# Kernel optimization log

Hardware: AMD Instinct MI355X
Metric: run time of the kernel (lower is better)

The kernel has to match this reference:

```python
import jax, jax.numpy as jnp
import numpy as np

EPS = 1e-20


def _conv(x, w, pad):
    # NCHW / OIHW conv, stride 1, symmetric padding
    return jax.lax.conv_general_dilated(
        x, w, window_strides=(1, 1),
        padding=((pad, pad), (pad, pad)),
        dimension_numbers=("NCHW", "OIHW", "NCHW"))


def _nconv(data, conf, w, b, pad):
    # normalized convolution: conv(d*c)/conv(c) + bias ; cout = conv(c)/sum(w)
    denom = _conv(conf, w, pad)
    nomin = _conv(data * conf, w, pad)
    out = nomin / (denom + EPS) + b[None, :, None, None]
    s = jnp.sum(w, axis=(1, 2, 3))  # per-out-channel kernel sum
    cout = denom / s[None, :, None, None]
    return out, cout


def _maxpool_ds(x, c):
    # 2x2/stride-2 max pool on c, gathering x at argmax positions (torch return_indices semantics)
    B, C, H, W = c.shape
    cw = c.reshape(B, C, H // 2, 2, W // 2, 2).transpose(0, 1, 2, 4, 3, 5).reshape(B, C, H // 2, W // 2, 4)
    xw = x.reshape(B, C, H // 2, 2, W // 2, 2).transpose(0, 1, 2, 4, 3, 5).reshape(B, C, H // 2, W // 2, 4)
    idx = jnp.argmax(cw, axis=-1)  # first-max tie-break, same as torch
    c_ds = jnp.take_along_axis(cw, idx[..., None], axis=-1)[..., 0] / 4.0
    x_ds = jnp.take_along_axis(xw, idx[..., None], axis=-1)[..., 0]
    return x_ds, c_ds


def _up2(x):
    return jnp.repeat(jnp.repeat(x, 2, axis=2), 2, axis=3)


def setup_inputs() -> dict:
    key = jax.random.key(0)
    ks = jax.random.split(key, 18)
    B, H, W = 8, 512, 512
    x0 = jax.random.normal(ks[0], (B, 1, H, W), dtype=jnp.float32)
    c0 = jax.random.uniform(ks[1], (B, 1, H, W), dtype=jnp.float32)

    def posw(k, shape):
        # positive kernel (the module enforces positivity via softplus hook)
        return jax.nn.softplus(jax.random.normal(k, shape, dtype=jnp.float32))

    inp = {"x0": x0, "c0": c0}
    shapes = {
        "w1": (2, 1, 5, 5), "w2": (2, 2, 5, 5), "w3": (2, 2, 5, 5),
        "w4": (2, 4, 3, 3), "w5": (2, 4, 3, 3), "w6": (2, 4, 3, 3),
        "w7": (1, 2, 1, 1),
    }
    for i, (name, shp) in enumerate(shapes.items()):
        inp[name] = posw(ks[2 + i], shp)
        inp["b" + name[1:]] = jnp.full((shp[0],), 0.01, dtype=jnp.float32)
    return inp


def reference(x0, c0, w1, b1, w2, b2, w3, b3, w4, b4, w5, b5, w6, b6, w7, b7):
    x1, c1 = _nconv(x0, c0, w1, b1, 2)
    x1, c1 = _nconv(x1, c1, w2, b2, 2)
    x1, c1 = _nconv(x1, c1, w3, b3, 2)

    x1_ds, c1_ds = _maxpool_ds(x1, c1)
    x2_ds, c2_ds = _nconv(x1_ds, c1_ds, w2, b2, 2)
    x2_ds, c2_ds = _nconv(x2_ds, c2_ds, w3, b3, 2)

    x2_dss, c2_dss = _maxpool_ds(x2_ds, c2_ds)
    x3_ds, c3_ds = _nconv(x2_dss, c2_dss, w2, b2, 2)

    x3_dss, c3_dss = _maxpool_ds(x3_ds, c3_ds)
    x4_ds, c4_ds = _nconv(x3_dss, c3_dss, w2, b2, 2)

    x4, c4 = _up2(x4_ds), _up2(c4_ds)
    x34_ds, c34_ds = _nconv(jnp.concatenate((x3_ds, x4), 1), jnp.concatenate((c3_ds, c4), 1), w4, b4, 1)

    x34, c34 = _up2(x34_ds), _up2(c34_ds)
    x23_ds, c23_ds = _nconv(jnp.concatenate((x2_ds, x34), 1), jnp.concatenate((c2_ds, c34), 1), w5, b5, 1)

    x23, c23 = _up2(x23_ds), _up2(c23_ds)
    xout, cout = _nconv(jnp.concatenate((x23, x1), 1), jnp.concatenate((c23, c1), 1), w6, b6, 1)
    xout, cout = _nconv(xout, cout, w7, b7, 0)
    return xout, cout
```

## Files before the change

### kernel.cpp

```cpp
#include <hip/hip_runtime.h>

#define EPSF 1e-20f

__device__ __forceinline__ float frcp(float x) { return __builtin_amdgcn_rcpf(x); }


template<int NCI, int CI0, int CINT, int K, int ROWS>
__device__ __forceinline__ void conv_core(const float* __restrict__ s_d,
                                          const float* __restrict__ s_c,
                                          const float* __restrict__ wgt,
                                          int lh, int lw,
                                          float den[2][4], float nom[2][4])
{
    constexpr int JOFF = 4 - (K / 2);
    #pragma unroll
    for (int kh = 0; kh < K; ++kh) {
        #pragma unroll
        for (int ci = 0; ci < NCI; ++ci) {
            const float2* rd = (const float2*)(s_d + (ci * ROWS + lh + kh) * 72 + lw + 2);
            const float2* rc = (const float2*)(s_c + (ci * ROWS + lh + kh) * 72 + lw + 2);
            float wd[8], wc[8];
            #pragma unroll
            for (int q = 0; q < 4; ++q) {
                const float2 t = rd[q];
                wd[2*q] = t.x; wd[2*q+1] = t.y;
                const float2 u = rc[q];
                wc[2*q] = u.x; wc[2*q+1] = u.y;
            }
            #pragma unroll
            for (int kw = 0; kw < K; ++kw) {
                const float w0 = wgt[((0 * CINT + CI0 + ci) * K + kh) * K + kw];
                const float w1 = wgt[((1 * CINT + CI0 + ci) * K + kh) * K + kw];
                #pragma unroll
                for (int p = 0; p < 4; ++p) {
                    const int j = p + kw + (JOFF - 2);
                    den[0][p] = fmaf(w0, wc[j], den[0][p]);
                    nom[0][p] = fmaf(w0, wd[j], nom[0][p]);
                    den[1][p] = fmaf(w1, wc[j], den[1][p]);
                    nom[1][p] = fmaf(w1, wd[j], nom[1][p]);
                }
            }
        }
    }
}

template<int LO0>
__device__ __forceinline__ void conv_low(const float* __restrict__ s_lo_d,
                                         const float* __restrict__ s_lo_c,
                                         const float* __restrict__ wgt,
                                         int lh, int lw,
                                         float den[2][4], float nom[2][4])
{
    #pragma unroll
    for (int kh = 0; kh < 3; ++kh) {
        const int rel_r = ((lh + kh - 1) >> 1) + 1;
        #pragma unroll
        for (int lci = 0; lci < 2; ++lci) {
            const float* rd = s_lo_d + (lci * 10 + rel_r) * 40 + (lw >> 1) + 2;
            const float* rc = s_lo_c + (lci * 10 + rel_r) * 40 + (lw >> 1) + 2;
            float wd[6], wc[6];
            #pragma unroll
            for (int q = 0; q < 3; ++q) {
                const float2 t = *(const float2*)(rd + 2 * q);
                wd[2*q] = t.x; wd[2*q+1] = t.y;
                const float2 u = *(const float2*)(rc + 2 * q);
                wc[2*q] = u.x; wc[2*q+1] = u.y;
            }
            #pragma unroll
            for (int kw = 0; kw < 3; ++kw) {
                const float w0 = wgt[((0 * 4 + LO0 + lci) * 3 + kh) * 3 + kw];
                const float w1 = wgt[((1 * 4 + LO0 + lci) * 3 + kh) * 3 + kw];
                #pragma unroll
                for (int p = 0; p < 4; ++p) {
                    const int t = p + kw - 1;
                    const int jl = ((t < 0) ? -1 : (t >> 1)) + 2;
                    den[0][p] = fmaf(w0, wc[jl], den[0][p]);
                    nom[0][p] = fmaf(w0, wd[jl], nom[0][p]);
                    den[1][p] = fmaf(w1, wc[jl], den[1][p]);
                    nom[1][p] = fmaf(w1, wd[jl], nom[1][p]);
                }
            }
        }
    }
}

template<int CINT, int K>
__device__ __forceinline__ void nconv_epilogue(const float* __restrict__ wgt,
                                               const float* __restrict__ bias,
                                               float den[2][4], float nom[2][4],
                                               float4 uo[2], float4 co4[2])
{
    #pragma unroll
    for (int c = 0; c < 2; ++c) {
        float s = 0.f;
        for (int i = 0; i < CINT * K * K; ++i) s += wgt[c * CINT * K * K + i];
        const float is = 1.0f / s;
        const float bb = bias[c];
        #pragma unroll
        for (int p = 0; p < 4; ++p) {
            const float xo = nom[c][p] * frcp(den[c][p] + EPSF) + bb;
            const float cv = den[c][p] * is;
            (&co4[c].x)[p] = cv;
            (&uo[c].x)[p]  = xo * cv;
        }
    }
}

__global__ __launch_bounds__(256)
void enc12_fused(const float* __restrict__ x0, const float* __restrict__ c0,
                 const float* __restrict__ wA, const float* __restrict__ bA,
                 const float* __restrict__ wB, const float* __restrict__ bB,
                 float* __restrict__ uout, float* __restrict__ cout)
{
    __shared__ __align__(16) float in_d[24][84], in_c[24][84];
    __shared__ __align__(16) float mid_d[2][20][72], mid_c[2][20][72];

    const int tid = threadIdx.x;
    const int bw = blockIdx.x * 64;
    const int bh = blockIdx.y * 16;
    const int b  = blockIdx.z;

    const float4* x4 = (const float4*)x0;
    const float4* c4 = (const float4*)c0;
    for (int i = tid; i < 480; i += 256) {
        const int r = i / 20, k = i % 20;
        const int gh = bh - 4 + r;
        const int gw4 = (bw >> 2) - 2 + k;
        float4 xx = make_float4(0.f, 0.f, 0.f, 0.f);
        float4 cc = make_float4(0.f, 0.f, 0.f, 0.f);
        if ((unsigned)gh < 512u && (unsigned)gw4 < 128u) {
            const int a = (b << 16) + (gh << 7) + gw4;
            xx = x4[a];
            cc = c4[a];
        }
        *(float4*)&in_d[r][4 * k] = make_float4(xx.x * cc.x, xx.y * cc.y, xx.z * cc.z, xx.w * cc.w);
        *(float4*)&in_c[r][4 * k] = cc;
    }

    float isA0, isA1;
    {
        float s0 = 0.f, s1 = 0.f;
        for (int i = 0; i < 25; ++i) { s0 += wA[i]; s1 += wA[25 + i]; }
        isA0 = 1.0f / s0;
        isA1 = 1.0f / s1;
    }
    __syncthreads();

    #pragma unroll
    for (int pass = 0; pass < 2; ++pass) {
        int r, g;
        bool active = true;
        if (pass == 0) { r = tid >> 4; g = tid & 15; }
        else {
            if (tid < 64) { r = 16 + (tid >> 4); g = tid & 15; }
            else if (tid < 104) { const int t = tid - 64; r = t >> 1; g = 16 + (t & 1); }
            else { active = false; r = 0; g = 0; }
        }
        if (active) {
            float den[2][4], nom[2][4];
            #pragma unroll
            for (int c = 0; c < 2; ++c)
                #pragma unroll
                for (int p = 0; p < 4; ++p) { den[c][p] = 0.f; nom[c][p] = 0.f; }
            #pragma unroll
            for (int kh = 0; kh < 5; ++kh) {
                const float2* rd = (const float2*)(&in_d[r + kh][4 * g + 2]);
                const float2* rc = (const float2*)(&in_c[r + kh][4 * g + 2]);
                float wd[8], wc[8];
                #pragma unroll
                for (int q = 0; q < 4; ++q) {
                    const float2 t = rd[q];
                    wd[2*q] = t.x; wd[2*q+1] = t.y;
                    const float2 u = rc[q];
                    wc[2*q] = u.x; wc[2*q+1] = u.y;
                }
                #pragma unroll
                for (int kw = 0; kw < 5; ++kw) {
                    const float w0 = wA[kh * 5 + kw];
                    const float w1 = wA[25 + kh * 5 + kw];
                    #pragma unroll
                    for (int p = 0; p < 4; ++p) {
                        const int m = p + kw;
                        den[0][p] = fmaf(w0, wc[m], den[0][p]);
                        nom[0][p] = fmaf(w0, wd[m], nom[0][p]);
                        den[1][p] = fmaf(w1, wc[m], den[1][p]);
                        nom[1][p] = fmaf(w1, wd[m], nom[1][p]);
                    }
                }
            }
            const int orow = bh + r - 2;
            const bool rok = (unsigned)orow < 512u;
            #pragma unroll
            for (int c = 0; c < 2; ++c) {
                const float is = (c == 0) ? isA0 : isA1;
                float4 du, dc;
                #pragma unroll
                for (int p = 0; p < 4; ++p) {
                    const int ocol = bw + 4 * g - 4 + p;
                    const bool ok = rok && (unsigned)ocol < 512u;
                    const float xo = nom[c][p] * frcp(den[c][p] + EPSF) + bA[c];
                    const float cv = den[c][p] * is;
                    (&dc.x)[p] = ok ? cv : 0.f;
                    (&du.x)[p] = ok ? xo * cv : 0.f;
                }
                *(float4*)&mid_d[c][r][4 * g] = du;
                *(float4*)&mid_c[c][r][4 * g] = dc;
            }
        }
    }
    __syncthreads();

    const int lh = tid >> 4;
    const int lw = (tid & 15) << 2;
    float den[2][4], nom[2][4];
    #pragma unroll
    for (int c = 0; c < 2; ++c)
        #pragma unroll
        for (int p = 0; p < 4; ++p) { den[c][p] = 0.f; nom[c][p] = 0.f; }

    conv_core<2, 0, 2, 5, 20>(&mid_d[0][0][0], &mid_c[0][0][0], wB, lh, lw, den, nom);

    float4 uo[2], co4[2];
    nconv_epilogue<2, 5>(wB, bB, den, nom, uo, co4);

    const int oh = bh + lh;
    #pragma unroll
    for (int c = 0; c < 2; ++c) {
        const int a = ((b * 2 + c) << 16) + (oh << 7) + ((bw + lw) >> 2);
        ((float4*)uout)[a] = uo[c];
        ((float4*)cout)[a] = co4[c];
    }
}

__global__ __launch_bounds__(256)
void enc45_fused(const float* __restrict__ inU, const float* __restrict__ inC,
                 const float* __restrict__ wA, const float* __restrict__ bA,
                 const float* __restrict__ wB, const float* __restrict__ bB,
                 float* __restrict__ uout, float* __restrict__ cout,
                 float* __restrict__ poolU, float* __restrict__ poolC)
{
    __shared__ __align__(16) float in_d[2][24][84], in_c[2][24][84];
    __shared__ __align__(16) float mid_d[2][20][72], mid_c[2][20][72];

    const int tid = threadIdx.x;
    const int bw = blockIdx.x * 64;
    const int bh = blockIdx.y * 16;
    const int b  = blockIdx.z;

    const float4* U4 = (const float4*)inU;
    const float4* C4 = (const float4*)inC;
    for (int i = tid; i < 960; i += 256) {
        const int ci = i / 480;
        const int r = (i / 20) % 24, k = i % 20;
        const int gh = bh - 4 + r;
        const int gw4 = (bw >> 2) - 2 + k;
        float4 dd = make_float4(0.f, 0.f, 0.f, 0.f);
        float4 cc = make_float4(0.f, 0.f, 0.f, 0.f);
        if ((unsigned)gh < 256u && (unsigned)gw4 < 64u) {
            const int a = ((b * 2 + ci) << 14) + (gh << 6) + gw4;
            dd = U4[a];
            cc = C4[a];
        }
        *(float4*)&in_d[ci][r][4 * k] = dd;
        *(float4*)&in_c[ci][r][4 * k] = cc;
    }

    float isA0, isA1;
    {
        float s0 = 0.f, s1 = 0.f;
        for (int i = 0; i < 50; ++i) { s0 += wA[i]; s1 += wA[50 + i]; }
        isA0 = 1.0f / s0;
        isA1 = 1.0f / s1;
    }
    __syncthreads();

    #pragma unroll
    for (int pass = 0; pass < 2; ++pass) {
        int r, g;
        bool active = true;
        if (pass == 0) { r = tid >> 4; g = tid & 15; }
        else {
            if (tid < 64) { r = 16 + (tid >> 4); g = tid & 15; }
            else if (tid < 104) { const int t = tid - 64; r = t >> 1; g = 16 + (t & 1); }
            else { active = false; r = 0; g = 0; }
        }
        if (active) {
            float den[2][4], nom[2][4];
            #pragma unroll
            for (int c = 0; c < 2; ++c)
                #pragma unroll
                for (int p = 0; p < 4; ++p) { den[c][p] = 0.f; nom[c][p] = 0.f; }
            #pragma unroll
            for (int kh = 0; kh < 5; ++kh) {
                #pragma unroll
                for (int ci = 0; ci < 2; ++ci) {
                    const float2* rd = (const float2*)(&in_d[ci][r + kh][4 * g + 2]);
                    const float2* rc = (const float2*)(&in_c[ci][r + kh][4 * g + 2]);
                    float wd[8], wc[8];
                    #pragma unroll
                    for (int q = 0; q < 4; ++q) {
                        const float2 t = rd[q];
                        wd[2*q] = t.x; wd[2*q+1] = t.y;
                        const float2 u = rc[q];
                        wc[2*q] = u.x; wc[2*q+1] = u.y;
                    }
                    #pragma unroll
                    for (int kw = 0; kw < 5; ++kw) {
                        const float w0 = wA[((0 * 2 + ci) * 5 + kh) * 5 + kw];
                        const float w1 = wA[((1 * 2 + ci) * 5 + kh) * 5 + kw];
                        #pragma unroll
                        for (int p = 0; p < 4; ++p) {
                            const int m = p + kw;
                            den[0][p] = fmaf(w0, wc[m], den[0][p]);
                            nom[0][p] = fmaf(w0, wd[m], nom[0][p]);
                            den[1][p] = fmaf(w1, wc[m], den[1][p]);
                            nom[1][p] = fmaf(w1, wd[m], nom[1][p]);
                        }
                    }
                }
            }
            const int orow = bh + r - 2;
            const bool rok = (unsigned)orow < 256u;
            #pragma unroll
            for (int c = 0; c < 2; ++c) {
                const float is = (c == 0) ? isA0 : isA1;
                float4 du, dc;
                #pragma unroll
                for (int p = 0; p < 4; ++p) {
                    const int ocol = bw + 4 * g - 4 + p;
                    const bool ok = rok && (unsigned)ocol < 256u;
                    const float xo = nom[c][p] * frcp(den[c][p] + EPSF) + bA[c];
                    const float cv = den[c][p] * is;
                    (&dc.x)[p] = ok ? cv : 0.f;
                    (&du.x)[p] = ok ? xo * cv : 0.f;
                }
                *(float4*)&mid_d[c][r][4 * g] = du;
                *(float4*)&mid_c[c][r][4 * g] = dc;
            }
        }
    }
    __syncthreads();

    const int lh = tid >> 4;
    const int lw = (tid & 15) << 2;
    float den[2][4], nom[2][4];
    #pragma unroll
    for (int c = 0; c < 2; ++c)
        #pragma unroll
        for (int p = 0; p < 4; ++p) { den[c][p] = 0.f; nom[c][p] = 0.f; }

    conv_core<2, 0, 2, 5, 20>(&mid_d[0][0][0], &mid_c[0][0][0], wB, lh, lw, den, nom);

    float4 uo[2], co4[2];
    nconv_epilogue<2, 5>(wB, bB, den, nom, uo, co4);

    const int oh = bh + lh;
    #pragma unroll
    for (int c = 0; c < 2; ++c) {
        const int a = ((b * 2 + c) << 14) + (oh << 6) + ((bw + lw) >> 2);
        ((float4*)uout)[a] = uo[c];
        ((float4*)cout)[a] = co4[c];
    }

    __syncthreads();
    float* pu = &mid_d[0][0][0];
    float* pcb = &mid_c[0][0][0];
    #pragma unroll
    for (int c = 0; c < 2; ++c) {
        *(float4*)&pu[(c * 16 + lh) * 64 + lw] = uo[c];
        *(float4*)&pcb[(c * 16 + lh) * 64 + lw] = co4[c];
    }
    __syncthreads();
    #pragma unroll
    for (int rep = 0; rep < 2; ++rep) {
        const int o = tid + rep * 256;
        const int ch = o >> 8;
        const int idx = o & 255;
        const int pr = idx >> 5;
        const int pcc = idx & 31;
        const int bse = (ch * 16 + 2 * pr) * 64 + 2 * pcc;
        const float c00 = pcb[bse],      c01 = pcb[bse + 1];
        const float c10 = pcb[bse + 64], c11 = pcb[bse + 65];
        float m = c00; float g = pu[bse];
        if (c01 > m) { m = c01; g = pu[bse + 1]; }
        if (c10 > m) { m = c10; g = pu[bse + 64]; }
        if (c11 > m) { m = c11; g = pu[bse + 65]; }
        const int pa = ((b * 2 + ch) << 14) + (((bh >> 1) + pr) << 7) + (bw >> 1) + pcc;
        poolU[pa] = g * 0.25f;
        poolC[pa] = m * 0.25f;
    }
}

__global__ __launch_bounds__(256)
void mid_kern(const float* __restrict__ p2U, const float* __restrict__ p2C,
              const float* __restrict__ w2, const float* __restrict__ b2,
              const float* __restrict__ w4, const float* __restrict__ b4,
              float* __restrict__ x34U, float* __restrict__ x34C)
{
    __shared__ __align__(16) float sp_d[2][32][88], sp_c[2][32][88];
    __shared__ __align__(16) float sx3_d[2][28][80], sx3_c[2][28][80];
    __shared__ __align__(16) float sp3_d[2][14][48], sp3_c[2][14][48];
    __shared__ __align__(16) float sx4_d[2][10][40], sx4_c[2][10][40];

    const int tid = threadIdx.x;
    const int bw = blockIdx.x * 64;
    const int bh = blockIdx.y * 16;
    const int b = blockIdx.z;

    const float4* U4 = (const float4*)p2U;
    const float4* C4 = (const float4*)p2C;
    for (int i = tid; i < 2 * 32 * 22; i += 256) {
        const int ci = i / 704;
        const int r  = (i / 22) % 32;
        const int cf = i % 22;
        const int gh = bh - 8 + r;
        const int gw4 = (bw >> 2) - 3 + cf;
        float4 dd = make_float4(0.f, 0.f, 0.f, 0.f);
        float4 cc = make_float4(0.f, 0.f, 0.f, 0.f);
        if ((unsigned)gh < 128u && (unsigned)gw4 < 32u) {
            const int a = ((b * 2 + ci) << 12) + (gh << 5) + gw4;
            dd = U4[a];
            cc = C4[a];
        }
        *(float4*)&sp_d[ci][r][cf * 4] = dd;
        *(float4*)&sp_c[ci][r][cf * 4] = cc;
    }
    __syncthreads();

    {
        float s2[2];
        #pragma unroll
        for (int c = 0; c < 2; ++c) {
            float s = 0.f;
            for (int i = 0; i < 50; ++i) s += w2[c * 50 + i];
            s2[c] = 1.0f / s;
        }
        for (int s = tid; s < 560; s += 256) {
            const int r = s / 20;
            const int g = s % 20;
            float den[2][4], nom[2][4];
            #pragma unroll
            for (int c = 0; c < 2; ++c)
                #pragma unroll
                for (int p = 0; p < 4; ++p) { den[c][p] = 0.f; nom[c][p] = 0.f; }
            #pragma unroll
            for (int kh = 0; kh < 5; ++kh) {
                #pragma unroll
                for (int ci = 0; ci < 2; ++ci) {
                    const float2* rd = (const float2*)(&sp_d[ci][r + kh][4 * g + 2]);
                    const float2* rc = (const float2*)(&sp_c[ci][r + kh][4 * g + 2]);
                    float wd[8], wc[8];
                    #pragma unroll
                    for (int q = 0; q < 4; ++q) {
                        const float2 t = rd[q];
                        wd[2*q] = t.x; wd[2*q+1] = t.y;
                        const float2 u = rc[q];
                        wc[2*q] = u.x; wc[2*q+1] = u.y;
                    }
                    #pragma unroll
                    for (int kw = 0; kw < 5; ++kw) {
                        const float w0 = w2[((0 * 2 + ci) * 5 + kh) * 5 + kw];
                        const float w1 = w2[((1 * 2 + ci) * 5 + kh) * 5 + kw];
                        #pragma unroll
                        for (int p = 0; p < 4; ++p) {
                            const int j = p + kw;
                            den[0][p] = fmaf(w0, wc[j], den[0][p]);
                            nom[0][p] = fmaf(w0, wd[j], nom[0][p]);
                            den[1][p] = fmaf(w1, wc[j], den[1][p]);
                            nom[1][p] = fmaf(w1, wd[j], nom[1][p]);
                        }
                    }
                }
            }
            const int orow = bh - 6 + r;
            const bool rok = (unsigned)orow < 128u;
            #pragma unroll
            for (int c = 0; c < 2; ++c) {
                float4 du, dc;
                #pragma unroll
                for (int p = 0; p < 4; ++p) {
                    const int ocol = bw - 8 + 4 * g + p;
                    const bool ok = rok && (unsigned)ocol < 128u;
                    const float xo = nom[c][p] * frcp(den[c][p] + EPSF) + b2[c];
                    const float cv = den[c][p] * s2[c];
                    (&dc.x)[p] = ok ? cv : 0.f;
                    (&du.x)[p] = ok ? xo * cv : 0.f;
                }
                *(float4*)&sx3_d[c][r][4 * g] = du;
                *(float4*)&sx3_c[c][r][4 * g] = dc;
            }
        }
    }
    __syncthreads();

    for (int i = tid; i < 2 * 14 * 48; i += 256) {
        const int ch = i / 672;
        const int r  = (i / 48) % 14;
        const int c  = i % 48;
        const int R = (bh >> 1) - 3 + r;
        const int C = (bw >> 1) - 8 + c;
        float g = 0.f, m = 0.f;
        if (c >= 4 && c < 44 && (unsigned)R < 64u && (unsigned)C < 64u) {
            const int xr = 2 * r, xc = 2 * c - 8;
            const float c00 = sx3_c[ch][xr][xc],     c01 = sx3_c[ch][xr][xc + 1];
            const float c10 = sx3_c[ch][xr + 1][xc], c11 = sx3_c[ch][xr + 1][xc + 1];
            m = c00; g = sx3_d[ch][xr][xc];
            if (c01 > m) { m = c01; g = sx3_d[ch][xr][xc + 1]; }
            if (c10 > m) { m = c10; g = sx3_d[ch][xr + 1][xc]; }
            if (c11 > m) { m = c11; g = sx3_d[ch][xr + 1][xc + 1]; }
            g *= 0.25f; m *= 0.25f;
        }
        sp3_d[ch][r][c] = g;
        sp3_c[ch][r][c] = m;
    }
    __syncthreads();

    {
        float s2[2];
        #pragma unroll
        for (int c = 0; c < 2; ++c) {
            float s = 0.f;
            for (int i = 0; i < 50; ++i) s += w2[c * 50 + i];
            s2[c] = 1.0f / s;
        }
        for (int s = tid; s < 100; s += 256) {
            const int r = s / 10;
            const int g = s % 10;
            float den[2][4], nom[2][4];
            #pragma unroll
            for (int c = 0; c < 2; ++c)
                #pragma unroll
                for (int p = 0; p < 4; ++p) { den[c][p] = 0.f; nom[c][p] = 0.f; }
            #pragma unroll
            for (int kh = 0; kh < 5; ++kh) {
                #pragma unroll
                for (int ci = 0; ci < 2; ++ci) {
                    const float2* rd = (const float2*)(&sp3_d[ci][r + kh][4 * g + 2]);
                    const float2* rc = (const float2*)(&sp3_c[ci][r + kh][4 * g + 2]);
                    float wd[8], wc[8];
                    #pragma unroll
                    for (int q = 0; q < 4; ++q) {
                        const float2 t = rd[q];
                        wd[2*q] = t.x; wd[2*q+1] = t.y;
                        const float2 u = rc[q];
                        wc[2*q] = u.x; wc[2*q+1] = u.y;
                    }
                    #pragma unroll
                    for (int kw = 0; kw < 5; ++kw) {
                        const float w0 = w2[((0 * 2 + ci) * 5 + kh) * 5 + kw];
                        const float w1 = w2[((1 * 2 + ci) * 5 + kh) * 5 + kw];
                        #pragma unroll
                        for (int p = 0; p < 4; ++p) {
                            const int j = p + kw;
                            den[0][p] = fmaf(w0, wc[j], den[0][p]);
                            nom[0][p] = fmaf(w0, wd[j], nom[0][p]);
                            den[1][p] = fmaf(w1, wc[j], den[1][p]);
                            nom[1][p] = fmaf(w1, wd[j], nom[1][p]);
                        }
                    }
                }
            }
            const int orow = (bh >> 1) - 1 + r;
            const bool rok = (unsigned)orow < 64u;
            #pragma unroll
            for (int c = 0; c < 2; ++c) {
                float4 du, dc;
                #pragma unroll
                for (int p = 0; p < 4; ++p) {
                    const int ocol = (bw >> 1) - 4 + 4 * g + p;
                    const bool ok = rok && (unsigned)ocol < 64u;
                    const float xo = nom[c][p] * frcp(den[c][p] + EPSF) + b2[c];
                    const float cv = den[c][p] * s2[c];
                    (&dc.x)[p] = ok ? cv : 0.f;
                    (&du.x)[p] = ok ? xo * cv : 0.f;
                }
                *(float4*)&sx4_d[c][r][4 * g] = du;
                *(float4*)&sx4_c[c][r][4 * g] = dc;
            }
        }
    }
    __syncthreads();

    {
        const int lh = tid >> 4;
        const int lw = (tid & 15) << 2;
        float den[2][4], nom[2][4];
        #pragma unroll
        for (int c = 0; c < 2; ++c)
            #pragma unroll
            for (int p = 0; p < 4; ++p) { den[c][p] = 0.f; nom[c][p] = 0.f; }

        #pragma unroll
        for (int kh = 0; kh < 3; ++kh) {
            #pragma unroll
            for (int ci = 0; ci < 2; ++ci) {
                const float2* rd = (const float2*)(&sx3_d[ci][lh + kh + 5][lw + 6]);
                const float2* rc = (const float2*)(&sx3_c[ci][lh + kh + 5][lw + 6]);
                float wd[8], wc[8];
                #pragma unroll
                for (int q = 0; q < 4; ++q) {
                    const float2 t = rd[q];
                    wd[2*q] = t.x; wd[2*q+1] = t.y;
                    const float2 u = rc[q];
                    wc[2*q] = u.x; wc[2*q+1] = u.y;
                }
                #pragma unroll
                for (int kw = 0; kw < 3; ++kw) {
                    const float w0 = w4[((0 * 4 + ci) * 3 + kh) * 3 + kw];
                    const float w1 = w4[((1 * 4 + ci) * 3 + kh) * 3 + kw];
                    #pragma unroll
                    for (int p = 0; p < 4; ++p) {
                        const int j = p + kw + 1;
                        den[0][p] = fmaf(w0, wc[j], den[0][p]);
                        nom[0][p] = fmaf(w0, wd[j], nom[0][p]);
                        den[1][p] = fmaf(w1, wc[j], den[1][p]);
                        nom[1][p] = fmaf(w1, wd[j], nom[1][p]);
                    }
                }
            }
        }
        conv_low<2>(&sx4_d[0][0][0], &sx4_c[0][0][0], w4, lh, lw, den, nom);

        float4 uo[2], co4[2];
        nconv_epilogue<4, 3>(w4, b4, den, nom, uo, co4);
        #pragma unroll
        for (int c = 0; c < 2; ++c) {
            const int a = ((b * 2 + c) << 12) + ((bh + lh) << 5) + ((bw + lw) >> 2);
            ((float4*)x34U)[a] = uo[c];
            ((float4*)x34C)[a] = co4[c];
        }
    }
}

template<int CIN, int K, int LOGHW, bool IN_IS_U, bool POOL>
__global__ __launch_bounds__(256)
void nconv_tiled(const float* __restrict__ xin, const float* __restrict__ cin_,
                 const float* __restrict__ wgt, const float* __restrict__ bias,
                 float* __restrict__ uout, float* __restrict__ cout,
                 float* __restrict__ poolU, float* __restrict__ poolC)
{
    constexpr int HW = 1 << LOGHW;
    constexpr int PAD = K / 2;
    constexpr int TH = 16;
    constexpr int ROWS = TH + 2 * PAD;
    constexpr int NC4 = 18;
    __shared__ __align__(16) float s_d[CIN][ROWS][72];
    __shared__ __align__(16) float s_c[CIN][ROWS][72];

    const int tid = threadIdx.x;
    const int base_w = blockIdx.x * 64;
    const int base_h = blockIdx.y * TH;
    const int b = blockIdx.z;

    constexpr int SLOTS = CIN * ROWS * NC4;
    const float4* x4 = (const float4*)xin;
    const float4* c4p = (const float4*)cin_;
    for (int i = tid; i < SLOTS; i += 256) {
        const int ci = i / (ROWS * NC4);
        const int r  = (i / NC4) % ROWS;
        const int cf = i % NC4;
        const int gh = base_h - PAD + r;
        const int gw4 = (base_w >> 2) + cf - 1;
        float4 dd = make_float4(0.f, 0.f, 0.f, 0.f);
        float4 cc = make_float4(0.f, 0.f, 0.f, 0.f);
        if ((unsigned)gh < (unsigned)HW && (unsigned)gw4 < (unsigned)(HW >> 2)) {
            const int a = ((b * CIN + ci) << (2 * LOGHW - 2)) + (gh << (LOGHW - 2)) + gw4;
            const float4 xx = x4[a];
            cc = c4p[a];
            if (IN_IS_U) dd = xx;
            else dd = make_float4(xx.x * cc.x, xx.y * cc.y, xx.z * cc.z, xx.w * cc.w);
        }
        *(float4*)&s_d[ci][r][cf * 4] = dd;
        *(float4*)&s_c[ci][r][cf * 4] = cc;
    }
    __syncthreads();

    const int lh = tid >> 4;
    const int lw = (tid & 15) << 2;
    float den[2][4], nom[2][4];
    #pragma unroll
    for (int c = 0; c < 2; ++c)
        #pragma unroll
        for (int p = 0; p < 4; ++p) { den[c][p] = 0.f; nom[c][p] = 0.f; }

    conv_core<CIN, 0, CIN, K, ROWS>(&s_d[0][0][0], &s_c[0][0][0], wgt, lh, lw, den, nom);

    float4 uo[2], co4[2];
    nconv_epilogue<CIN, K>(wgt, bias, den, nom, uo, co4);

    const int oh = base_h + lh;
    #pragma unroll
    for (int c = 0; c < 2; ++c) {
        const int a = ((b * 2 + c) << (2 * LOGHW - 2)) + (oh << (LOGHW - 2)) + ((base_w + lw) >> 2);
        ((float4*)uout)[a] = uo[c];
        ((float4*)cout)[a] = co4[c];
    }

    if (POOL) {
        __syncthreads();
        float* pu = &s_d[0][0][0];
        float* pcb = &s_c[0][0][0];
        #pragma unroll
        for (int c = 0; c < 2; ++c) {
            *(float4*)&pu[(c * 16 + lh) * 64 + lw] = uo[c];
            *(float4*)&pcb[(c * 16 + lh) * 64 + lw] = co4[c];
        }
        __syncthreads();
        #pragma unroll
        for (int rep = 0; rep < 2; ++rep) {
            const int o = tid + rep * 256;
            const int ch = o >> 8;
            const int idx = o & 255;
            const int pr = idx >> 5;
            const int pcc = idx & 31;
            const int bse = (ch * 16 + 2 * pr) * 64 + 2 * pcc;
            const float c00 = pcb[bse],      c01 = pcb[bse + 1];
            const float c10 = pcb[bse + 64], c11 = pcb[bse + 65];
            float m = c00; float g = pu[bse];
            if (c01 > m) { m = c01; g = pu[bse + 1]; }
            if (c10 > m) { m = c10; g = pu[bse + 64]; }
            if (c11 > m) { m = c11; g = pu[bse + 65]; }
            const int pa = ((b * 2 + ch) << (2 * (LOGHW - 1)))
                         + (((base_h >> 1) + pr) << (LOGHW - 1)) + (base_w >> 1) + pcc;
            poolU[pa] = g * 0.25f;
            poolC[pa] = m * 0.25f;
        }
    }
}

template<bool UP_FIRST, int LOGHW, bool FINAL>
__global__ __launch_bounds__(256)
void nconv_cat_tiled(const float* __restrict__ skU, const float* __restrict__ skC,
                     const float* __restrict__ loU, const float* __restrict__ loC,
                     const float* __restrict__ wgt, const float* __restrict__ bias,
                     float* __restrict__ uout, float* __restrict__ cout,
                     const float* __restrict__ w7, const float* __restrict__ b7)
{
    constexpr int HW = 1 << LOGHW;
    constexpr int HWL = HW >> 1;
    constexpr int TH = 16;
    constexpr int ROWS = TH + 2;
    constexpr int NC4 = 18;
    constexpr int SK0 = UP_FIRST ? 2 : 0;
    constexpr int LO0 = UP_FIRST ? 0 : 2;
    __shared__ __align__(16) float s_d[2][ROWS][72];
    __shared__ __align__(16) float s_c[2][ROWS][72];
    __shared__ __align__(16) float s_lo_d[2][10][40];
    __shared__ __align__(16) float s_lo_c[2][10][40];

    const int tid = threadIdx.x;
    const int base_w = blockIdx.x * 64;
    const int base_h = blockIdx.y * TH;
    const int b = blockIdx.z;

    constexpr int SLOTS = 2 * ROWS * NC4;
    const float4* sU4 = (const float4*)skU;
    const float4* sC4 = (const float4*)skC;
    for (int i = tid; i < SLOTS; i += 256) {
        const int ci = i / (ROWS * NC4);
        const int r  = (i / NC4) % ROWS;
        const int cf = i % NC4;
        const int gh = base_h - 1 + r;
        const int gw4 = (base_w >> 2) + cf - 1;
        float4 dd = make_float4(0.f, 0.f, 0.f, 0.f);
        float4 cc = make_float4(0.f, 0.f, 0.f, 0.f);
        if ((unsigned)gh < (unsigned)HW && (unsigned)gw4 < (unsigned)(HW >> 2)) {
            const int a = ((b * 2 + ci) << (2 * LOGHW - 2)) + (gh << (LOGHW - 2)) + gw4;
            dd = sU4[a];
            cc = sC4[a];
        }
        *(float4*)&s_d[ci][r][cf * 4] = dd;
        *(float4*)&s_c[ci][r][cf * 4] = cc;
    }
    constexpr int LO_SLOTS = 2 * 10 * 10;
    const int lo_r0 = (base_h >> 1) - 1;
    const int lo_c4_0 = (base_w >> 3) - 1;
    const float4* lU4 = (const float4*)loU;
    const float4* lC4 = (const float4*)loC;
    for (int i = tid; i < LO_SLOTS; i += 256) {
        const int ci = i / 100;
        const int r  = (i / 10) % 10;
        const int cf = i % 10;
        const int gr = lo_r0 + r;
        const int gc4 = lo_c4_0 + cf;
        float4 dd = make_float4(0.f, 0.f, 0.f, 0.f);
        float4 cc = make_float4(0.f, 0.f, 0.f, 0.f);
        if ((unsigned)gr < (unsigned)HWL && (unsigned)gc4 < (unsigned)(HWL >> 2)) {
            const int a = ((b * 2 + ci) << (2 * (LOGHW - 1) - 2)) + (gr << (LOGHW - 3)) + gc4;
            dd = lU4[a];
            cc = lC4[a];
        }
        *(float4*)&s_lo_d[ci][r][cf * 4] = dd;
        *(float4*)&s_lo_c[ci][r][cf * 4] = cc;
    }
    __syncthreads();

    const int lh = tid >> 4;
    const int lw = (tid & 15) << 2;
    float den[2][4], nom[2][4];
    #pragma unroll
    for (int c = 0; c < 2; ++c)
        #pragma unroll
        for (int p = 0; p < 4; ++p) { den[c][p] = 0.f; nom[c][p] = 0.f; }

    conv_core<2, SK0, 4, 3, ROWS>(&s_d[0][0][0], &s_c[0][0][0], wgt, lh, lw, den, nom);
    conv_low<LO0>(&s_lo_d[0][0][0], &s_lo_c[0][0][0], wgt, lh, lw, den, nom);

    float4 uo[2], co4[2];
    nconv_epilogue<4, 3>(wgt, bias, den, nom, uo, co4);

    const int oh = base_h + lh;
    if (FINAL) {
        const float w70 = w7[0], w71 = w7[1], bb7 = b7[0];
        const float inv = frcp(w70 + w71);
        float4 xo4, cc4;
        #pragma unroll
        for (int p = 0; p < 4; ++p) {
            const float d1 = w70 * (&co4[0].x)[p] + w71 * (&co4[1].x)[p];
            (&xo4.x)[p] = (w70 * (&uo[0].x)[p] + w71 * (&uo[1].x)[p]) * frcp(d1 + EPSF) + bb7;
            (&cc4.x)[p] = d1 * inv;
        }
        const int a = (b << (2 * LOGHW - 2)) + (oh << (LOGHW - 2)) + ((base_w + lw) >> 2);
        ((float4*)uout)[a] = xo4;
        ((float4*)uout)[(1 << 19) + a] = cc4;
    } else {
        #pragma unroll
        for (int c = 0; c < 2; ++c) {
            const int a = ((b * 2 + c) << (2 * LOGHW - 2)) + (oh << (LOGHW - 2)) + ((base_w + lw) >> 2);
            ((float4*)uout)[a] = uo[c];
            ((float4*)cout)[a] = co4[c];
        }
    }
}

extern "C" void kernel_launch(void* const* d_in, const int* in_sizes, int n_in,
                              void* d_out, int out_size, void* d_ws, size_t ws_size,
                              hipStream_t stream) {
    (void)in_sizes; (void)n_in; (void)out_size; (void)ws_size;
    const float* x0 = (const float*)d_in[0];
    const float* c0 = (const float*)d_in[1];
    const float* w1 = (const float*)d_in[2];  const float* b1 = (const float*)d_in[3];
    const float* w2 = (const float*)d_in[4];  const float* b2 = (const float*)d_in[5];
    const float* w3 = (const float*)d_in[6];  const float* b3 = (const float*)d_in[7];
    const float* w4 = (const float*)d_in[8];  const float* b4 = (const float*)d_in[9];
    const float* w5 = (const float*)d_in[10]; const float* b5 = (const float*)d_in[11];
    const float* w6 = (const float*)d_in[12]; const float* b6 = (const float*)d_in[13];
    const float* w7 = (const float*)d_in[14]; const float* b7 = (const float*)d_in[15];

    float* ws = (float*)d_ws;
    const size_t S512 = 8ull * 2 * 512 * 512;
    const size_t S256 = 8ull * 2 * 256 * 256;
    const size_t S128 = 8ull * 2 * 128 * 128;

    float* X1x = ws;            float* X1c = ws + S512;
    float* Ax  = ws + 2 * S512; float* Ac  = ws + 3 * S512;
    float* Bx  = ws + 4 * S512; float* Bc  = ws + 5 * S512;
    float* x23x = Ax;               float* x23c = Ax + S256;
    float* x2x  = Ax + 2 * S256;    float* x2c  = Ax + 3 * S256;
    float* p1x  = Ax + 4 * S256;    float* p1c  = Ax + 5 * S256;
    float* p2x  = Bx + 2 * S128;    float* p2c  = Bx + 3 * S128;
    float* x34x = Bx + 4 * S128;    float* x34c = Bx + 5 * S128;

    enc12_fused<<<dim3(8, 32, 8), 256, 0, stream>>>(
        x0, c0, w1, b1, w2, b2, Bx, Bc);
    nconv_tiled<2, 5, 9, true, true><<<dim3(8, 32, 8), 256, 0, stream>>>(
        Bx, Bc, w3, b3, X1x, X1c, p1x, p1c);
    enc45_fused<<<dim3(4, 16, 8), 256, 0, stream>>>(
        p1x, p1c, w2, b2, w3, b3, x2x, x2c, p2x, p2c);
    mid_kern<<<dim3(2, 8, 8), 256, 0, stream>>>(
        p2x, p2c, w2, b2, w4, b4, x34x, x34c);
    nconv_cat_tiled<false, 8, false><<<dim3(4, 16, 8), 256, 0, stream>>>(
        x2x, x2c, x34x, x34c, w5, b5, x23x, x23c, nullptr, nullptr);
    nconv_cat_tiled<true, 9, true><<<dim3(8, 32, 8), 256, 0, stream>>>(
        X1x, X1c, x23x, x23c, w6, b6, (float*)d_out, nullptr, w7, b7);
}
```

Before: 142.1 us.

## Interleave confidence and data into float2 shared-memory tiles across all conv kernels

Replaces the separate shared-memory arrays for confidence and confidence-weighted data with one interleaved float2 array per tile. Window loads become four 16-byte LDS reads per row instead of eight 8-byte reads, and accumulators are kept as float2 pairs (den, nom), which may let the compiler emit packed FMA. The pooling stage also reads interleaved pairs. Shared-memory footprint is unchanged, but bank-conflict patterns and register allocation shift, so occupancy may change.

```diff
diff --git a/kernel.cpp b/kernel.cpp
--- a/kernel.cpp
+++ b/kernel.cpp
@@ -5,39 +5,53 @@
 __device__ __forceinline__ float frcp(float x) { return __builtin_amdgcn_rcpf(x); }
 
 
+struct CD8 { float2 v[8]; };
+__device__ __forceinline__ CD8 load_cd8(const float2* p) {
+    const float4* q = (const float4*)p;
+    const float4 t0 = q[0], t1 = q[1], t2 = q[2], t3 = q[3];
+    CD8 r;
+    r.v[0] = make_float2(t0.x, t0.y); r.v[1] = make_float2(t0.z, t0.w);
+    r.v[2] = make_float2(t1.x, t1.y); r.v[3] = make_float2(t1.z, t1.w);
+    r.v[4] = make_float2(t2.x, t2.y); r.v[5] = make_float2(t2.z, t2.w);
+    r.v[6] = make_float2(t3.x, t3.y); r.v[7] = make_float2(t3.z, t3.w);
+    return r;
+}
+struct CD6 { float2 v[6]; };
+__device__ __forceinline__ CD6 load_cd6(const float2* p) {
+    const float4* q = (const float4*)p;
+    const float4 t0 = q[0], t1 = q[1], t2 = q[2];
+    CD6 r;
+    r.v[0] = make_float2(t0.x, t0.y); r.v[1] = make_float2(t0.z, t0.w);
+    r.v[2] = make_float2(t1.x, t1.y); r.v[3] = make_float2(t1.z, t1.w);
+    r.v[4] = make_float2(t2.x, t2.y); r.v[5] = make_float2(t2.z, t2.w);
+    return r;
+}
+__device__ __forceinline__ void fma2(float2& a, float w, float2 cd) {
+    a.x = fmaf(w, cd.x, a.x);
+    a.y = fmaf(w, cd.y, a.y);
+}
+
 template<int NCI, int CI0, int CINT, int K, int ROWS>
-__device__ __forceinline__ void conv_core(const float* __restrict__ s_d,
-                                          const float* __restrict__ s_c,
-                                          const float* __restrict__ wgt,
-                                          int lh, int lw,
-                                          float den[2][4], float nom[2][4])
+__device__ __forceinline__ void conv_core_i(const float2* __restrict__ s,
+                                            const float* __restrict__ wgt,
+                                            int lh, int lw,
+                                            float2 acc[2][4])
 {
-    constexpr int JOFF = 4 - (K / 2);
+    constexpr int JB = 2 - (K / 2);
     #pragma unroll
     for (int kh = 0; kh < K; ++kh) {
         #pragma unroll
         for (int ci = 0; ci < NCI; ++ci) {
-            const float2* rd = (const float2*)(s_d + (ci * ROWS + lh + kh) * 72 + lw + 2);
-            const float2* rc = (const float2*)(s_c + (ci * ROWS + lh + kh) * 72 + lw + 2);
-            float wd[8], wc[8];
-            #pragma unroll
-            for (int q = 0; q < 4; ++q) {
-                const float2 t = rd[q];
-                wd[2*q] = t.x; wd[2*q+1] = t.y;
-                const float2 u = rc[q];
-                wc[2*q] = u.x; wc[2*q+1] = u.y;
-            }
+            const CD8 cd = load_cd8(s + (ci * ROWS + lh + kh) * 72 + lw + 2);
             #pragma unroll
             for (int kw = 0; kw < K; ++kw) {
                 const float w0 = wgt[((0 * CINT + CI0 + ci) * K + kh) * K + kw];
                 const float w1 = wgt[((1 * CINT + CI0 + ci) * K + kh) * K + kw];
                 #pragma unroll
                 for (int p = 0; p < 4; ++p) {
-                    const int j = p + kw + (JOFF - 2);
-                    den[0][p] = fmaf(w0, wc[j], den[0][p]);
-                    nom[0][p] = fmaf(w0, wd[j], nom[0][p]);
-                    den[1][p] = fmaf(w1, wc[j], den[1][p]);
-                    nom[1][p] = fmaf(w1, wd[j], nom[1][p]);
+                    const int j = p + kw + JB;
+                    fma2(acc[0][p], w0, cd.v[j]);
+                    fma2(acc[1][p], w1, cd.v[j]);
                 }
             }
         }
@@ -45,27 +59,17 @@
 }
 
 template<int LO0>
-__device__ __forceinline__ void conv_low(const float* __restrict__ s_lo_d,
-                                         const float* __restrict__ s_lo_c,
-                                         const float* __restrict__ wgt,
-                                         int lh, int lw,
-                                         float den[2][4], float nom[2][4])
+__device__ __forceinline__ void conv_low_i(const float2* __restrict__ s_lo,
+                                           const float* __restrict__ wgt,
+                                           int lh, int lw,
+                                           float2 acc[2][4])
 {
     #pragma unroll
     for (int kh = 0; kh < 3; ++kh) {
         const int rel_r = ((lh + kh - 1) >> 1) + 1;
         #pragma unroll
         for (int lci = 0; lci < 2; ++lci) {
-            const float* rd = s_lo_d + (lci * 10 + rel_r) * 40 + (lw >> 1) + 2;
-            const float* rc = s_lo_c + (lci * 10 + rel_r) * 40 + (lw >> 1) + 2;
-            float wd[6], wc[6];
-            #pragma unroll
-            for (int q = 0; q < 3; ++q) {
-                const float2 t = *(const float2*)(rd + 2 * q);
-                wd[2*q] = t.x; wd[2*q+1] = t.y;
-                const float2 u = *(const float2*)(rc + 2 * q);
-                wc[2*q] = u.x; wc[2*q+1] = u.y;
-            }
+            const CD6 cd = load_cd6(s_lo + (lci * 10 + rel_r) * 40 + (lw >> 1) + 2);
             #pragma unroll
             for (int kw = 0; kw < 3; ++kw) {
                 const float w0 = wgt[((0 * 4 + LO0 + lci) * 3 + kh) * 3 + kw];
@@ -74,10 +78,8 @@
                 for (int p = 0; p < 4; ++p) {
                     const int t = p + kw - 1;
                     const int jl = ((t < 0) ? -1 : (t >> 1)) + 2;
-                    den[0][p] = fmaf(w0, wc[jl], den[0][p]);
-                    nom[0][p] = fmaf(w0, wd[jl], nom[0][p]);
-                    den[1][p] = fmaf(w1, wc[jl], den[1][p]);
-                    nom[1][p] = fmaf(w1, wd[jl], nom[1][p]);
+                    fma2(acc[0][p], w0, cd.v[jl]);
+                    fma2(acc[1][p], w1, cd.v[jl]);
                 }
             }
         }
@@ -85,10 +87,10 @@
 }
 
 template<int CINT, int K>
-__device__ __forceinline__ void nconv_epilogue(const float* __restrict__ wgt,
-                                               const float* __restrict__ bias,
-                                               float den[2][4], float nom[2][4],
-                                               float4 uo[2], float4 co4[2])
+__device__ __forceinline__ void nconv_epilogue_i(const float* __restrict__ wgt,
+                                                 const float* __restrict__ bias,
+                                                 float2 acc[2][4],
+                                                 float4 uo[2], float4 co4[2])
 {
     #pragma unroll
     for (int c = 0; c < 2; ++c) {
@@ -98,8 +100,8 @@
         const float bb = bias[c];
         #pragma unroll
         for (int p = 0; p < 4; ++p) {
-            const float xo = nom[c][p] * frcp(den[c][p] + EPSF) + bb;
-            const float cv = den[c][p] * is;
+            const float xo = acc[c][p].y * frcp(acc[c][p].x + EPSF) + bb;
+            const float cv = acc[c][p].x * is;
             (&co4[c].x)[p] = cv;
             (&uo[c].x)[p]  = xo * cv;
         }
@@ -112,8 +114,8 @@
                  const float* __restrict__ wB, const float* __restrict__ bB,
                  float* __restrict__ uout, float* __restrict__ cout)
 {
-    __shared__ __align__(16) float in_d[24][84], in_c[24][84];
-    __shared__ __align__(16) float mid_d[2][20][72], mid_c[2][20][72];
+    __shared__ __align__(16) float2 in_cd[24][84];
+    __shared__ __align__(16) float2 mid_cd[2][20][72];
 
     const int tid = threadIdx.x;
     const int bw = blockIdx.x * 64;
@@ -133,8 +135,9 @@
             xx = x4[a];
             cc = c4[a];
         }
-        *(float4*)&in_d[r][4 * k] = make_float4(xx.x * cc.x, xx.y * cc.y, xx.z * cc.z, xx.w * cc.w);
-        *(float4*)&in_c[r][4 * k] = cc;
+        float4* dst = (float4*)&in_cd[r][4 * k];
+        dst[0] = make_float4(cc.x, xx.x * cc.x, cc.y, xx.y * cc.y);
+        dst[1] = make_float4(cc.z, xx.z * cc.z, cc.w, xx.w * cc.w);
     }
 
     float isA0, isA1;
@@ -157,34 +160,22 @@
             else { active = false; r = 0; g = 0; }
         }
         if (active) {
-            float den[2][4], nom[2][4];
+            float2 acc[2][4];
             #pragma unroll
             for (int c = 0; c < 2; ++c)
                 #pragma unroll
-                for (int p = 0; p < 4; ++p) { den[c][p] = 0.f; nom[c][p] = 0.f; }
+                for (int p = 0; p < 4; ++p) acc[c][p] = make_float2(0.f, 0.f);
             #pragma unroll
             for (int kh = 0; kh < 5; ++kh) {
-                const float2* rd = (const float2*)(&in_d[r + kh][4 * g + 2]);
-                const float2* rc = (const float2*)(&in_c[r + kh][4 * g + 2]);
-                float wd[8], wc[8];
-                #pragma unroll
-                for (int q = 0; q < 4; ++q) {
-                    const float2 t = rd[q];
-                    wd[2*q] = t.x; wd[2*q+1] = t.y;
-                    const float2 u = rc[q];
-                    wc[2*q] = u.x; wc[2*q+1] = u.y;
-                }
+                const CD8 cd = load_cd8(&in_cd[r + kh][4 * g + 2]);
                 #pragma unroll
                 for (int kw = 0; kw < 5; ++kw) {
                     const float w0 = wA[kh * 5 + kw];
                     const float w1 = wA[25 + kh * 5 + kw];
                     #pragma unroll
                     for (int p = 0; p < 4; ++p) {
-                        const int m = p + kw;
-                        den[0][p] = fmaf(w0, wc[m], den[0][p]);
-                        nom[0][p] = fmaf(w0, wd[m], nom[0][p]);
-                        den[1][p] = fmaf(w1, wc[m], den[1][p]);
-                        nom[1][p] = fmaf(w1, wd[m], nom[1][p]);
+                        fma2(acc[0][p], w0, cd.v[p + kw]);
+                        fma2(acc[1][p], w1, cd.v[p + kw]);
                     }
                 }
             }
@@ -193,18 +184,19 @@
             #pragma unroll
             for (int c = 0; c < 2; ++c) {
                 const float is = (c == 0) ? isA0 : isA1;
-                float4 du, dc;
+                float cv[4], du[4];
                 #pragma unroll
                 for (int p = 0; p < 4; ++p) {
                     const int ocol = bw + 4 * g - 4 + p;
                     const bool ok = rok && (unsigned)ocol < 512u;
-                    const float xo = nom[c][p] * frcp(den[c][p] + EPSF) + bA[c];
-                    const float cv = den[c][p] * is;
-                    (&dc.x)[p] = ok ? cv : 0.f;
-                    (&du.x)[p] = ok ? xo * cv : 0.f;
-                }
-                *(float4*)&mid_d[c][r][4 * g] = du;
-                *(float4*)&mid_c[c][r][4 * g] = dc;
+                    const float xo = acc[c][p].y * frcp(acc[c][p].x + EPSF) + bA[c];
+                    const float v = acc[c][p].x * is;
+                    cv[p] = ok ? v : 0.f;
+                    du[p] = ok ? xo * v : 0.f;
+                }
+                float4* dst = (float4*)&mid_cd[c][r][4 * g];
+                dst[0] = make_float4(cv[0], du[0], cv[1], du[1]);
+                dst[1] = make_float4(cv[2], du[2], cv[3], du[3]);
             }
         }
     }
@@ -212,16 +204,16 @@
 
     const int lh = tid >> 4;
     const int lw = (tid & 15) << 2;
-    float den[2][4], nom[2][4];
+    float2 acc[2][4];
     #pragma unroll
     for (int c = 0; c < 2; ++c)
         #pragma unroll
-        for (int p = 0; p < 4; ++p) { den[c][p] = 0.f; nom[c][p] = 0.f; }
-
-    conv_core<2, 0, 2, 5, 20>(&mid_d[0][0][0], &mid_c[0][0][0], wB, lh, lw, den, nom);
+        for (int p = 0; p < 4; ++p) acc[c][p] = make_float2(0.f, 0.f);
+
+    conv_core_i<2, 0, 2, 5, 20>(&mid_cd[0][0][0], wB, lh, lw, acc);
 
     float4 uo[2], co4[2];
-    nconv_epilogue<2, 5>(wB, bB, den, nom, uo, co4);
+    nconv_epilogue_i<2, 5>(wB, bB, acc, uo, co4);
 
     const int oh = bh + lh;
     #pragma unroll
@@ -239,8 +231,8 @@
                  float* __restrict__ uout, float* __restrict__ cout,
                  float* __restrict__ poolU, float* __restrict__ poolC)
 {
-    __shared__ __align__(16) float in_d[2][24][84], in_c[2][24][84];
-    __shared__ __align__(16) float mid_d[2][20][72], mid_c[2][20][72];
+    __shared__ __align__(16) float2 in_cd[2][24][84];
+    __shared__ __align__(16) float2 mid_cd[2][20][72];
 
     const int tid = threadIdx.x;
     const int bw = blockIdx.x * 64;
@@ -261,8 +253,9 @@
             dd = U4[a];
             cc = C4[a];
         }
-        *(float4*)&in_d[ci][r][4 * k] = dd;
-        *(float4*)&in_c[ci][r][4 * k] = cc;
+        float4* dst = (float4*)&in_cd[ci][r][4 * k];
+        dst[0] = make_float4(cc.x, dd.x, cc.y, dd.y);
+        dst[1] = make_float4(cc.z, dd.z, cc.w, dd.w);
     }
 
     float isA0, isA1;
@@ -285,36 +278,24 @@
             else { active = false; r = 0; g = 0; }
         }
         if (active) {
-            float den[2][4], nom[2][4];
+            float2 acc[2][4];
             #pragma unroll
             for (int c = 0; c < 2; ++c)
                 #pragma unroll
-                for (int p = 0; p < 4; ++p) { den[c][p] = 0.f; nom[c][p] = 0.f; }
+                for (int p = 0; p < 4; ++p) acc[c][p] = make_float2(0.f, 0.f);
             #pragma unroll
             for (int kh = 0; kh < 5; ++kh) {
                 #pragma unroll
                 for (int ci = 0; ci < 2; ++ci) {
-                    const float2* rd = (const float2*)(&in_d[ci][r + kh][4 * g + 2]);
-                    const float2* rc = (const float2*)(&in_c[ci][r + kh][4 * g + 2]);
-                    float wd[8], wc[8];
-                    #pragma unroll
-                    for (int q = 0; q < 4; ++q) {
-                        const float2 t = rd[q];
-                        wd[2*q] = t.x; wd[2*q+1] = t.y;
-                        const float2 u = rc[q];
-                        wc[2*q] = u.x; wc[2*q+1] = u.y;
-                    }
+                    const CD8 cd = load_cd8(&in_cd[ci][r + kh][4 * g + 2]);
                     #pragma unroll
                     for (int kw = 0; kw < 5; ++kw) {
                         const float w0 = wA[((0 * 2 + ci) * 5 + kh) * 5 + kw];
                         const float w1 = wA[((1 * 2 + ci) * 5 + kh) * 5 + kw];
                         #pragma unroll
                         for (int p = 0; p < 4; ++p) {
-                            const int m = p + kw;
-                            den[0][p] = fmaf(w0, wc[m], den[0][p]);
-                            nom[0][p] = fmaf(w0, wd[m], nom[0][p]);
-                            den[1][p] = fmaf(w1, wc[m], den[1][p]);
-                            nom[1][p] = fmaf(w1, wd[m], nom[1][p]);
+                            fma2(acc[0][p], w0, cd.v[p + kw]);
+                            fma2(acc[1][p], w1, cd.v[p + kw]);
                         }
                     }
                 }
@@ -324,18 +305,19 @@
             #pragma unroll
             for (int c = 0; c < 2; ++c) {
                 const float is = (c == 0) ? isA0 : isA1;
-                float4 du, dc;
+                float cv[4], du[4];
                 #pragma unroll
                 for (int p = 0; p < 4; ++p) {
                     const int ocol = bw + 4 * g - 4 + p;
                     const bool ok = rok && (unsigned)ocol < 256u;
-                    const float xo = nom[c][p] * frcp(den[c][p] + EPSF) + bA[c];
-                    const float cv = den[c][p] * is;
-                    (&dc.x)[p] = ok ? cv : 0.f;
-                    (&du.x)[p] = ok ? xo * cv : 0.f;
-                }
-                *(float4*)&mid_d[c][r][4 * g] = du;
-                *(float4*)&mid_c[c][r][4 * g] = dc;
+                    const float xo = acc[c][p].y * frcp(acc[c][p].x + EPSF) + bA[c];
+                    const float v = acc[c][p].x * is;
+                    cv[p] = ok ? v : 0.f;
+                    du[p] = ok ? xo * v : 0.f;
+                }
+                float4* dst = (float4*)&mid_cd[c][r][4 * g];
+                dst[0] = make_float4(cv[0], du[0], cv[1], du[1]);
+                dst[1] = make_float4(cv[2], du[2], cv[3], du[3]);
             }
         }
     }
@@ -343,16 +325,16 @@
 
     const int lh = tid >> 4;
     const int lw = (tid & 15) << 2;
-    float den[2][4], nom[2][4];
+    float2 acc[2][4];
     #pragma unroll
     for (int c = 0; c < 2; ++c)
         #pragma unroll
-        for (int p = 0; p < 4; ++p) { den[c][p] = 0.f; nom[c][p] = 0.f; }
-
-    conv_core<2, 0, 2, 5, 20>(&mid_d[0][0][0], &mid_c[0][0][0], wB, lh, lw, den, nom);
+        for (int p = 0; p < 4; ++p) acc[c][p] = make_float2(0.f, 0.f);
+
+    conv_core_i<2, 0, 2, 5, 20>(&mid_cd[0][0][0], wB, lh, lw, acc);
 
     float4 uo[2], co4[2];
-    nconv_epilogue<2, 5>(wB, bB, den, nom, uo, co4);
+    nconv_epilogue_i<2, 5>(wB, bB, acc, uo, co4);
 
     const int oh = bh + lh;
     #pragma unroll
@@ -363,12 +345,13 @@
     }
 
     __syncthreads();
-    float* pu = &mid_d[0][0][0];
-    float* pcb = &mid_c[0][0][0];
+    float2* pb = &mid_cd[0][0][0];
     #pragma unroll
     for (int c = 0; c < 2; ++c) {
-        *(float4*)&pu[(c * 16 + lh) * 64 + lw] = uo[c];
-        *(float4*)&pcb[(c * 16 + lh) * 64 + lw] = co4[c];
+        float2* row = pb + (c * 16 + lh) * 64 + lw;
+        #pragma unroll
+        for (int p = 0; p < 4; ++p)
+            row[p] = make_float2((&co4[c].x)[p], (&uo[c].x)[p]);
     }
     __syncthreads();
     #pragma unroll
@@ -378,13 +361,12 @@
         const int idx = o & 255;
         const int pr = idx >> 5;
         const int pcc = idx & 31;
-        const int bse = (ch * 16 + 2 * pr) * 64 + 2 * pcc;
-        const float c00 = pcb[bse],      c01 = pcb[bse + 1];
-        const float c10 = pcb[bse + 64], c11 = pcb[bse + 65];
-        float m = c00; float g = pu[bse];
-        if (c01 > m) { m = c01; g = pu[bse + 1]; }
-        if (c10 > m) { m = c10; g = pu[bse + 64]; }
-        if (c11 > m) { m = c11; g = pu[bse + 65]; }
+        const float2* base = pb + (ch * 16 + 2 * pr) * 64 + 2 * pcc;
+        const float2 a0 = base[0], a1 = base[1], a2 = base[64], a3 = base[65];
+        float m = a0.x, g = a0.y;
+        if (a1.x > m) { m = a1.x; g = a1.y; }
+        if (a2.x > m) { m = a2.x; g = a2.y; }
+        if (a3.x > m) { m = a3.x; g = a3.y; }
         const int pa = ((b * 2 + ch) << 14) + (((bh >> 1) + pr) << 7) + (bw >> 1) + pcc;
         poolU[pa] = g * 0.25f;
         poolC[pa] = m * 0.25f;
@@ -397,10 +379,10 @@
               const float* __restrict__ w4, const float* __restrict__ b4,
               float* __restrict__ x34U, float* __restrict__ x34C)
 {
-    __shared__ __align__(16) float sp_d[2][32][88], sp_c[2][32][88];
-    __shared__ __align__(16) float sx3_d[2][28][80], sx3_c[2][28][80];
-    __shared__ __align__(16) float sp3_d[2][14][48], sp3_c[2][14][48];
-    __shared__ __align__(16) float sx4_d[2][10][40], sx4_c[2][10][40];
+    __shared__ __align__(16) float2 sp_cd[2][32][88];
+    __shared__ __align__(16) float2 sx3_cd[2][28][80];
+    __shared__ __align__(16) float2 sp3_cd[2][14][48];
+    __shared__ __align__(16) float2 sx4_cd[2][10][40];
 
     const int tid = threadIdx.x;
     const int bw = blockIdx.x * 64;
@@ -422,8 +404,9 @@
             dd = U4[a];
             cc = C4[a];
         }
-        *(float4*)&sp_d[ci][r][cf * 4] = dd;
-        *(float4*)&sp_c[ci][r][cf * 4] = cc;
+        float4* dst = (float4*)&sp_cd[ci][r][cf * 4];
+        dst[0] = make_float4(cc.x, dd.x, cc.y, dd.y);
+        dst[1] = make_float4(cc.z, dd.z, cc.w, dd.w);
     }
     __syncthreads();
 
@@ -438,36 +421,24 @@
         for (int s = tid; s < 560; s += 256) {
             const int r = s / 20;
             const int g = s % 20;
-            float den[2][4], nom[2][4];
+            float2 acc[2][4];
             #pragma unroll
             for (int c = 0; c < 2; ++c)
                 #pragma unroll
-                for (int p = 0; p < 4; ++p) { den[c][p] = 0.f; nom[c][p] = 0.f; }
+                for (int p = 0; p < 4; ++p) acc[c][p] = make_float2(0.f, 0.f);
             #pragma unroll
             for (int kh = 0; kh < 5; ++kh) {
                 #pragma unroll
                 for (int ci = 0; ci < 2; ++ci) {
-                    const float2* rd = (const float2*)(&sp_d[ci][r + kh][4 * g + 2]);
-                    const float2* rc = (const float2*)(&sp_c[ci][r + kh][4 * g + 2]);
-                    float wd[8], wc[8];
-                    #pragma unroll
-                    for (int q = 0; q < 4; ++q) {
-                        const float2 t = rd[q];
-                        wd[2*q] = t.x; wd[2*q+1] = t.y;
-                        const float2 u = rc[q];
-                        wc[2*q] = u.x; wc[2*q+1] = u.y;
-                    }
+                    const CD8 cd = load_cd8(&sp_cd[ci][r + kh][4 * g + 2]);
                     #pragma unroll
                     for (int kw = 0; kw < 5; ++kw) {
                         const float w0 = w2[((0 * 2 + ci) * 5 + kh) * 5 + kw];
                         const float w1 = w2[((1 * 2 + ci) * 5 + kh) * 5 + kw];
                         #pragma unroll
                         for (int p = 0; p < 4; ++p) {
-                            const int j = p + kw;
-                            den[0][p] = fmaf(w0, wc[j], den[0][p]);
-                            nom[0][p] = fmaf(w0, wd[j], nom[0][p]);
-                            den[1][p] = fmaf(w1, wc[j], den[1][p]);
-                            nom[1][p] = fmaf(w1, wd[j], nom[1][p]);
+                            fma2(acc[0][p], w0, cd.v[p + kw]);
+                            fma2(acc[1][p], w1, cd.v[p + kw]);
                         }
                     }
                 }
@@ -476,18 +447,19 @@
             const bool rok = (unsigned)orow < 128u;
             #pragma unroll
             for (int c = 0; c < 2; ++c) {
-                float4 du, dc;
+                float cv[4], du[4];
                 #pragma unroll
                 for (int p = 0; p < 4; ++p) {
                     const int ocol = bw - 8 + 4 * g + p;
                     const bool ok = rok && (unsigned)ocol < 128u;
-                    const float xo = nom[c][p] * frcp(den[c][p] + EPSF) + b2[c];
-                    const float cv = den[c][p] * s2[c];
-                    (&dc.x)[p] = ok ? cv : 0.f;
-                    (&du.x)[p] = ok ? xo * cv : 0.f;
-                }
-                *(float4*)&sx3_d[c][r][4 * g] = du;
-                *(float4*)&sx3_c[c][r][4 * g] = dc;
+                    const float xo = acc[c][p].y * frcp(acc[c][p].x + EPSF) + b2[c];
+                    const float v = acc[c][p].x * s2[c];
+                    cv[p] = ok ? v : 0.f;
+                    du[p] = ok ? xo * v : 0.f;
+                }
+                float4* dst = (float4*)&sx3_cd[c][r][4 * g];
+                dst[0] = make_float4(cv[0], du[0], cv[1], du[1]);
+                dst[1] = make_float4(cv[2], du[2], cv[3], du[3]);
             }
         }
     }
@@ -502,16 +474,15 @@
         float g = 0.f, m = 0.f;
         if (c >= 4 && c < 44 && (unsigned)R < 64u && (unsigned)C < 64u) {
             const int xr = 2 * r, xc = 2 * c - 8;
-            const float c00 = sx3_c[ch][xr][xc],     c01 = sx3_c[ch][xr][xc + 1];
-            const float c10 = sx3_c[ch][xr + 1][xc], c11 = sx3_c[ch][xr + 1][xc + 1];
-            m = c00; g = sx3_d[ch][xr][xc];
-            if (c01 > m) { m = c01; g = sx3_d[ch][xr][xc + 1]; }
-            if (c10 > m) { m = c10; g = sx3_d[ch][xr + 1][xc]; }
-            if (c11 > m) { m = c11; g = sx3_d[ch][xr + 1][xc + 1]; }
+            const float2 a0 = sx3_cd[ch][xr][xc],     a1 = sx3_cd[ch][xr][xc + 1];
+            const float2 a2 = sx3_cd[ch][xr + 1][xc], a3 = sx3_cd[ch][xr + 1][xc + 1];
+            m = a0.x; g = a0.y;
+            if (a1.x > m) { m = a1.x; g = a1.y; }
+            if (a2.x > m) { m = a2.x; g = a2.y; }
+            if (a3.x > m) { m = a3.x; g = a3.y; }
             g *= 0.25f; m *= 0.25f;
         }
-        sp3_d[ch][r][c] = g;
-        sp3_c[ch][r][c] = m;
+        sp3_cd[ch][r][c] = make_float2(m, g);
     }
     __syncthreads();
 
@@ -526,36 +497,24 @@
         for (int s = tid; s < 100; s += 256) {
             const int r = s / 10;
             const int g = s % 10;
-            float den[2][4], nom[2][4];
+            float2 acc[2][4];
             #pragma unroll
             for (int c = 0; c < 2; ++c)
                 #pragma unroll
-                for (int p = 0; p < 4; ++p) { den[c][p] = 0.f; nom[c][p] = 0.f; }
+                for (int p = 0; p < 4; ++p) acc[c][p] = make_float2(0.f, 0.f);
             #pragma unroll
             for (int kh = 0; kh < 5; ++kh) {
                 #pragma unroll
                 for (int ci = 0; ci < 2; ++ci) {
-                    const float2* rd = (const float2*)(&sp3_d[ci][r + kh][4 * g + 2]);
-                    const float2* rc = (const float2*)(&sp3_c[ci][r + kh][4 * g + 2]);
-                    float wd[8], wc[8];
-                    #pragma unroll
-                    for (int q = 0; q < 4; ++q) {
-                        const float2 t = rd[q];
-                        wd[2*q] = t.x; wd[2*q+1] = t.y;
-                        const float2 u = rc[q];
-                        wc[2*q] = u.x; wc[2*q+1] = u.y;
-                    }
+                    const CD8 cd = load_cd8(&sp3_cd[ci][r + kh][4 * g + 2]);
                     #pragma unroll
                     for (int kw = 0; kw < 5; ++kw) {
                         const float w0 = w2[((0 * 2 + ci) * 5 + kh) * 5 + kw];
                         const float w1 = w2[((1 * 2 + ci) * 5 + kh) * 5 + kw];
                         #pragma unroll
                         for (int p = 0; p < 4; ++p) {
-                            const int j = p + kw;
-                            den[0][p] = fmaf(w0, wc[j], den[0][p]);
-                            nom[0][p] = fmaf(w0, wd[j], nom[0][p]);
-                            den[1][p] = fmaf(w1, wc[j], den[1][p]);
-                            nom[1][p] = fmaf(w1, wd[j], nom[1][p]);
+                            fma2(acc[0][p], w0, cd.v[p + kw]);
+                            fma2(acc[1][p], w1, cd.v[p + kw]);
                         }
                     }
                 }
@@ -564,18 +523,19 @@
             const bool rok = (unsigned)orow < 64u;
             #pragma unroll
             for (int c = 0; c < 2; ++c) {
-                float4 du, dc;
+                float cv[4], du[4];
                 #pragma unroll
                 for (int p = 0; p < 4; ++p) {
                     const int ocol = (bw >> 1) - 4 + 4 * g + p;
                     const bool ok = rok && (unsigned)ocol < 64u;
-                    const float xo = nom[c][p] * frcp(den[c][p] + EPSF) + b2[c];
-                    const float cv = den[c][p] * s2[c];
-                    (&dc.x)[p] = ok ? cv : 0.f;
-                    (&du.x)[p] = ok ? xo * cv : 0.f;
-                }
-                *(float4*)&sx4_d[c][r][4 * g] = du;
-                *(float4*)&sx4_c[c][r][4 * g] = dc;
+                    const float xo = acc[c][p].y * frcp(acc[c][p].x + EPSF) + b2[c];
+                    const float v = acc[c][p].x * s2[c];
+                    cv[p] = ok ? v : 0.f;
+                    du[p] = ok ? xo * v : 0.f;
+                }
+                float4* dst = (float4*)&sx4_cd[c][r][4 * g];
+                dst[0] = make_float4(cv[0], du[0], cv[1], du[1]);
+                dst[1] = make_float4(cv[2], du[2], cv[3], du[3]);
             }
         }
     }
@@ -584,26 +544,17 @@
     {
         const int lh = tid >> 4;
         const int lw = (tid & 15) << 2;
-        float den[2][4], nom[2][4];
+        float2 acc[2][4];
         #pragma unroll
         for (int c = 0; c < 2; ++c)
             #pragma unroll
-            for (int p = 0; p < 4; ++p) { den[c][p] = 0.f; nom[c][p] = 0.f; }
+            for (int p = 0; p < 4; ++p) acc[c][p] = make_float2(0.f, 0.f);
 
         #pragma unroll
         for (int kh = 0; kh < 3; ++kh) {
             #pragma unroll
             for (int ci = 0; ci < 2; ++ci) {
-                const float2* rd = (const float2*)(&sx3_d[ci][lh + kh + 5][lw + 6]);
-                const float2* rc = (const float2*)(&sx3_c[ci][lh + kh + 5][lw + 6]);
-                float wd[8], wc[8];
-                #pragma unroll
-                for (int q = 0; q < 4; ++q) {
-                    const float2 t = rd[q];
-                    wd[2*q] = t.x; wd[2*q+1] = t.y;
-                    const float2 u = rc[q];
-                    wc[2*q] = u.x; wc[2*q+1] = u.y;
-                }
+                const CD8 cd = load_cd8(&sx3_cd[ci][lh + kh + 5][lw + 6]);
                 #pragma unroll
                 for (int kw = 0; kw < 3; ++kw) {
                     const float w0 = w4[((0 * 4 + ci) * 3 + kh) * 3 + kw];
@@ -611,18 +562,16 @@
                     #pragma unroll
                     for (int p = 0; p < 4; ++p) {
                         const int j = p + kw + 1;
-                        den[0][p] = fmaf(w0, wc[j], den[0][p]);
-                        nom[0][p] = fmaf(w0, wd[j], nom[0][p]);
-                        den[1][p] = fmaf(w1, wc[j], den[1][p]);
-                        nom[1][p] = fmaf(w1, wd[j], nom[1][p]);
+                        fma2(acc[0][p], w0, cd.v[j]);
+                        fma2(acc[1][p], w1, cd.v[j]);
                     }
                 }
             }
         }
-        conv_low<2>(&sx4_d[0][0][0], &sx4_c[0][0][0], w4, lh, lw, den, nom);
+        conv_low_i<2>(&sx4_cd[0][0][0], w4, lh, lw, acc);
 
         float4 uo[2], co4[2];
-        nconv_epilogue<4, 3>(w4, b4, den, nom, uo, co4);
+        nconv_epilogue_i<4, 3>(w4, b4, acc, uo, co4);
         #pragma unroll
         for (int c = 0; c < 2; ++c) {
             const int a = ((b * 2 + c) << 12) + ((bh + lh) << 5) + ((bw + lw) >> 2);
@@ -644,8 +593,7 @@
     constexpr int TH = 16;
     constexpr int ROWS = TH + 2 * PAD;
     constexpr int NC4 = 18;
-    __shared__ __align__(16) float s_d[CIN][ROWS][72];
-    __shared__ __align__(16) float s_c[CIN][ROWS][72];
+    __shared__ __align__(16) float2 s_cd[CIN][ROWS][72];
 
     const int tid = threadIdx.x;
     const int base_w = blockIdx.x * 64;
@@ -670,23 +618,24 @@
             if (IN_IS_U) dd = xx;
             else dd = make_float4(xx.x * cc.x, xx.y * cc.y, xx.z * cc.z, xx.w * cc.w);
         }
-        *(float4*)&s_d[ci][r][cf * 4] = dd;
-        *(float4*)&s_c[ci][r][cf * 4] = cc;
+        float4* dst = (float4*)&s_cd[ci][r][cf * 4];
+        dst[0] = make_float4(cc.x, dd.x, cc.y, dd.y);
+        dst[1] = make_float4(cc.z, dd.z, cc.w, dd.w);
     }
     __syncthreads();
 
     const int lh = tid >> 4;
     const int lw = (tid & 15) << 2;
-    float den[2][4], nom[2][4];
+    float2 acc[2][4];
     #pragma unroll
     for (int c = 0; c < 2; ++c)
         #pragma unroll
-        for (int p = 0; p < 4; ++p) { den[c][p] = 0.f; nom[c][p] = 0.f; }
-
-    conv_core<CIN, 0, CIN, K, ROWS>(&s_d[0][0][0], &s_c[0][0][0], wgt, lh, lw, den, nom);
+        for (int p = 0; p < 4; ++p) acc[c][p] = make_float2(0.f, 0.f);
+
+    conv_core_i<CIN, 0, CIN, K, ROWS>(&s_cd[0][0][0], wgt, lh, lw, acc);
 
     float4 uo[2], co4[2];
-    nconv_epilogue<CIN, K>(wgt, bias, den, nom, uo, co4);
+    nconv_epilogue_i<CIN, K>(wgt, bias, acc, uo, co4);
 
     const int oh = base_h + lh;
     #pragma unroll
@@ -698,12 +647,13 @@
 
     if (POOL) {
         __syncthreads();
-        float* pu = &s_d[0][0][0];
-        float* pcb = &s_c[0][0][0];
+        float2* pb = &s_cd[0][0][0];
         #pragma unroll
         for (int c = 0; c < 2; ++c) {
-            *(float4*)&pu[(c * 16 + lh) * 64 + lw] = uo[c];
-            *(float4*)&pcb[(c * 16 + lh) * 64 + lw] = co4[c];
+            float2* row = pb + (c * 16 + lh) * 64 + lw;
+            #pragma unroll
+            for (int p = 0; p < 4; ++p)
+                row[p] = make_float2((&co4[c].x)[p], (&uo[c].x)[p]);
         }
         __syncthreads();
         #pragma unroll
@@ -713,13 +663,12 @@
             const int idx = o & 255;
             const int pr = idx >> 5;
             const int pcc = idx & 31;
-            const int bse = (ch * 16 + 2 * pr) * 64 + 2 * pcc;
-            const float c00 = pcb[bse],      c01 = pcb[bse + 1];
-            const float c10 = pcb[bse + 64], c11 = pcb[bse + 65];
-            float m = c00; float g = pu[bse];
-            if (c01 > m) { m = c01; g = pu[bse + 1]; }
-            if (c10 > m) { m = c10; g = pu[bse + 64]; }
-            if (c11 > m) { m = c11; g = pu[bse + 65]; }
+            const float2* base = pb + (ch * 16 + 2 * pr) * 64 + 2 * pcc;
+            const float2 a0 = base[0], a1 = base[1], a2 = base[64], a3 = base[65];
+            float m = a0.x, g = a0.y;
+            if (a1.x > m) { m = a1.x; g = a1.y; }
+            if (a2.x > m) { m = a2.x; g = a2.y; }
+            if (a3.x > m) { m = a3.x; g = a3.y; }
             const int pa = ((b * 2 + ch) << (2 * (LOGHW - 1)))
                          + (((base_h >> 1) + pr) << (LOGHW - 1)) + (base_w >> 1) + pcc;
             poolU[pa] = g * 0.25f;
@@ -743,10 +692,8 @@
     constexpr int NC4 = 18;
     constexpr int SK0 = UP_FIRST ? 2 : 0;
     constexpr int LO0 = UP_FIRST ? 0 : 2;
-    __shared__ __align__(16) float s_d[2][ROWS][72];
-    __shared__ __align__(16) float s_c[2][ROWS][72];
-    __shared__ __align__(16) float s_lo_d[2][10][40];
-    __shared__ __align__(16) float s_lo_c[2][10][40];
+    __shared__ __align__(16) float2 s_cd[2][ROWS][72];
+    __shared__ __align__(16) float2 lo_cd[2][10][40];
 
     const int tid = threadIdx.x;
     const int base_w = blockIdx.x * 64;
@@ -769,8 +716,9 @@
             dd = sU4[a];
             cc = sC4[a];
         }
-        *(float4*)&s_d[ci][r][cf * 4] = dd;
-        *(float4*)&s_c[ci][r][cf * 4] = cc;
+        float4* dst = (float4*)&s_cd[ci][r][cf * 4];
+        dst[0] = make_float4(cc.x, dd.x, cc.y, dd.y);
+        dst[1] = make_float4(cc.z, dd.z, cc.w, dd.w);
     }
     constexpr int LO_SLOTS = 2 * 10 * 10;
     const int lo_r0 = (base_h >> 1) - 1;
@@ -790,24 +738,25 @@
             dd = lU4[a];
             cc = lC4[a];
         }
-        *(float4*)&s_lo_d[ci][r][cf * 4] = dd;
-        *(float4*)&s_lo_c[ci][r][cf * 4] = cc;
+        float4* dst = (float4*)&lo_cd[ci][r][cf * 4];
+        dst[0] = make_float4(cc.x, dd.x, cc.y, dd.y);
+        dst[1] = make_float4(cc.z, dd.z, cc.w, dd.w);
     }
     __syncthreads();
 
     const int lh = tid >> 4;
     const int lw = (tid & 15) << 2;
-    float den[2][4], nom[2][4];
+    float2 acc[2][4];
     #pragma unroll
     for (int c = 0; c < 2; ++c)
         #pragma unroll
-        for (int p = 0; p < 4; ++p) { den[c][p] = 0.f; nom[c][p] = 0.f; }
-
-    conv_core<2, SK0, 4, 3, ROWS>(&s_d[0][0][0], &s_c[0][0][0], wgt, lh, lw, den, nom);
-    conv_low<LO0>(&s_lo_d[0][0][0], &s_lo_c[0][0][0], wgt, lh, lw, den, nom);
+        for (int p = 0; p < 4; ++p) acc[c][p] = make_float2(0.f, 0.f);
+
+    conv_core_i<2, SK0, 4, 3, ROWS>(&s_cd[0][0][0], wgt, lh, lw, acc);
+    conv_low_i<LO0>(&lo_cd[0][0][0], wgt, lh, lw, acc);
 
     float4 uo[2], co4[2];
-    nconv_epilogue<4, 3>(wgt, bias, den, nom, uo, co4);
+    nconv_epilogue_i<4, 3>(wgt, bias, acc, uo, co4);
 
     const int oh = base_h + lh;
     if (FINAL) {
```

Result: faster. 125.7 us (-11.5%).
